# Kernel tuning notes

Measured on AMD Instinct MI355X. Metric: run time of the kernel, lower is better.

The kernel has to match this reference:

```python
import jax, jax.numpy as jnp
import numpy as np

EPS = 1e-5  # torch default for InstanceNorm2d and BatchNorm2d
B, C, H, W = 16, 128, 8192, 1


def _instance_norm(x):
    # normalize over spatial dims (H, W) per sample, per channel; affine=False (torch default)
    mean = jnp.mean(x, axis=(2, 3), keepdims=True)
    var = jnp.var(x, axis=(2, 3), keepdims=True)
    return (x - mean) * jax.lax.rsqrt(var + EPS)


def _batch_norm(x, gamma, beta):
    # training-mode batch norm: stats over (B, H, W) per channel, affine transform
    mean = jnp.mean(x, axis=(0, 2, 3), keepdims=True)
    var = jnp.var(x, axis=(0, 2, 3), keepdims=True)
    xn = (x - mean) * jax.lax.rsqrt(var + EPS)
    return xn * gamma[None, :, None, None] + beta[None, :, None, None]


def _block(x, g, be, w, b):
    # InstanceNorm -> BatchNorm -> ReLU -> 1x1 Conv
    x = jax.nn.relu(_batch_norm(_instance_norm(x), g, be))
    return jnp.einsum('bchw,oc->bohw', x, w) + b[None, :, None, None]


def setup_inputs() -> dict:
    key = jax.random.key(0)
    ks = jax.random.split(key, 6)
    return {
        'Correlation_feats': jax.random.normal(ks[0], (B, C, H, W), jnp.float32),
        'Coherence_residual_feats': jax.random.normal(ks[1], (B, C, H, W), jnp.float32),
        'feats': jax.random.normal(ks[2], (B, C, H, W), jnp.float32),
        'fc_w': jax.random.normal(ks[3], (2 * C,), jnp.float32) * 0.05,
        'fc_b': jnp.zeros((1,), jnp.float32),
        'w1': jax.random.normal(ks[4], (C, C), jnp.float32) * (1.0 / np.sqrt(C)),
        'b1': jnp.zeros((C,), jnp.float32),
        'g1': jnp.ones((C,), jnp.float32),
        'be1': jnp.zeros((C,), jnp.float32),
        'w2': jax.random.normal(ks[5], (C, C), jnp.float32) * (1.0 / np.sqrt(C)),
        'b2': jnp.zeros((C,), jnp.float32),
        'g2': jnp.ones((C,), jnp.float32),
        'be2': jnp.zeros((C,), jnp.float32),
    }


def reference(Correlation_feats, Coherence_residual_feats, feats,
              fc_w, fc_b, w1, b1, g1, be1, w2, b2, g2, be2):
    # pre_defined_alpha is None branch: alpha = sigmoid(fc(cat(Corr, Coh)))
    cat = jnp.concatenate([Correlation_feats, Coherence_residual_feats], axis=1)  # [B,2C,H,W]
    logit = jnp.einsum('bchw,c->bhw', cat, fc_w)[:, None, :, :] + fc_b[0]  # [B,1,H,W]
    alpha = jax.nn.sigmoid(logit)
    agg = Correlation_feats - alpha * feats
    x = _block(agg, g1, be1, w1, b1)
    x = _block(x, g2, be2, w2, b2)
    return x
```

## Files before the change

kernel.cpp:

```cpp
#include <hip/hip_runtime.h>

#define NB 16
#define NC 128
#define NH 8192
#define EPSN 1e-5f

typedef __attribute__((ext_vector_type(8))) short short8;
typedef __attribute__((ext_vector_type(4))) float f32x4;

__device__ inline unsigned short f2bf(float f) {
  unsigned int u = __builtin_bit_cast(unsigned int, f);
  u = u + 0x7FFFu + ((u >> 16) & 1u);
  return (unsigned short)(u >> 16);
}

__global__ __launch_bounds__(256) void alpha_kernel(
    const float* __restrict__ corr, const float* __restrict__ coh,
    const float* __restrict__ fcw, const float* __restrict__ fcb,
    float* __restrict__ alpha) {
  int idx = blockIdx.x * 256 + threadIdx.x;
  int b = idx >> 13;
  int h = idx & (NH - 1);
  const float* pc = corr + ((size_t)b * NC) * NH + h;
  const float* ph = coh + ((size_t)b * NC) * NH + h;
  float a0 = 0.f, a1 = 0.f, a2 = 0.f, a3 = 0.f;
#pragma unroll 8
  for (int c = 0; c < NC; c += 4) {
    a0 = fmaf(pc[(size_t)(c + 0) * NH], fcw[c + 0], a0);
    a1 = fmaf(pc[(size_t)(c + 1) * NH], fcw[c + 1], a1);
    a2 = fmaf(pc[(size_t)(c + 2) * NH], fcw[c + 2], a2);
    a3 = fmaf(pc[(size_t)(c + 3) * NH], fcw[c + 3], a3);
  }
#pragma unroll 8
  for (int c = 0; c < NC; c += 4) {
    a0 = fmaf(ph[(size_t)(c + 0) * NH], fcw[NC + c + 0], a0);
    a1 = fmaf(ph[(size_t)(c + 1) * NH], fcw[NC + c + 1], a1);
    a2 = fmaf(ph[(size_t)(c + 2) * NH], fcw[NC + c + 2], a2);
    a3 = fmaf(ph[(size_t)(c + 3) * NH], fcw[NC + c + 3], a3);
  }
  float l = (a0 + a1) + (a2 + a3) + fcb[0];
  alpha[idx] = 1.0f / (1.0f + __expf(-l));
}

__global__ __launch_bounds__(256) void agg_kernel(
    const float* __restrict__ corr, const float* __restrict__ feats,
    const float* __restrict__ alpha, float* __restrict__ agg,
    float* __restrict__ stats) {
  int blk = blockIdx.x;
  int chunk = blk & 3;
  int bc = blk >> 2;
  int b = bc >> 7;
  size_t base = (size_t)bc * NH + chunk * 2048;
  const float* pa = alpha + (size_t)b * NH + chunk * 2048;
  int t = threadIdx.x;
  float s = 0.f, q = 0.f;
#pragma unroll
  for (int r = 0; r < 2; ++r) {
    int off = r * 1024 + t * 4;
    float4 cv = *(const float4*)(corr + base + off);
    float4 fv = *(const float4*)(feats + base + off);
    float4 av = *(const float4*)(pa + off);
    float4 g;
    g.x = cv.x - av.x * fv.x;
    g.y = cv.y - av.y * fv.y;
    g.z = cv.z - av.z * fv.z;
    g.w = cv.w - av.w * fv.w;
    *(float4*)(agg + base + off) = g;
    s += (g.x + g.y) + (g.z + g.w);
    q = fmaf(g.x, g.x, q);
    q = fmaf(g.y, g.y, q);
    q = fmaf(g.z, g.z, q);
    q = fmaf(g.w, g.w, q);
  }
#pragma unroll
  for (int m = 32; m >= 1; m >>= 1) {
    s += __shfl_xor(s, m);
    q += __shfl_xor(q, m);
  }
  __shared__ float red[8];
  int wid = t >> 6;
  if ((t & 63) == 0) {
    red[wid * 2] = s;
    red[wid * 2 + 1] = q;
  }
  __syncthreads();
  if (t == 0) {
    float S = (red[0] + red[2]) + (red[4] + red[6]);
    float Q = (red[1] + red[3]) + (red[5] + red[7]);
    atomicAdd(&stats[bc * 2], S);
    atomicAdd(&stats[bc * 2 + 1], Q);
  }
}

__global__ void finalize_kernel(const float* __restrict__ stats,
                                const float* __restrict__ g,
                                const float* __restrict__ be,
                                float* __restrict__ scale,
                                float* __restrict__ shift) {
  int c = threadIdx.x;
  float mean[NB], rstd[NB];
  float bnacc = 0.f;
#pragma unroll
  for (int b = 0; b < NB; ++b) {
    float s = stats[(b * NC + c) * 2];
    float q = stats[(b * NC + c) * 2 + 1];
    float m = s * (1.f / NH);
    float v = fmaxf(q * (1.f / NH) - m * m, 0.f);
    float r = rsqrtf(v + EPSN);
    mean[b] = m;
    rstd[b] = r;
    bnacc += v * r * r;
  }
  float bnr = rsqrtf(bnacc * (1.f / NB) + EPSN);
  float gc = g[c], bec = be[c];
#pragma unroll
  for (int b = 0; b < NB; ++b) {
    float sc = rstd[b] * bnr * gc;
    scale[b * NC + c] = sc;
    shift[b * NC + c] = fmaf(-mean[b], sc, bec);
  }
}

template <bool DOSTATS>
__global__ __launch_bounds__(256) void conv_mfma_kernel(
    const float* X, const float* __restrict__ scale,
    const float* __restrict__ shift, const float* __restrict__ W,
    const float* __restrict__ bias, float* Out, float* __restrict__ stats) {
  __shared__ __align__(16) unsigned short sXf[8192];
  __shared__ float ssum[NC], ssq[NC];
  const int t = threadIdx.x;
  const int b = blockIdx.x >> 5;
  const int hbase = (blockIdx.x & 31) << 8;
  const int lane = t & 63;
  const int wv = t >> 6;
  const int wo = wv >> 1;
  const int wh = wv & 1;

  if (DOSTATS && t < NC) { ssum[t] = 0.f; ssq[t] = 0.f; }

  const int cb = (t >> 4) << 3;
  const int hq = t & 15;
  const int fragw = ((hq >> 2) << 2) + (cb >> 5);
  const int sub0 = (((cb >> 3) & 3) << 4) + ((hq & 3) << 2);
  const unsigned swz = ((unsigned)(sub0 >> 3)) << 4;
  const unsigned br = ((unsigned)(lane << 4)) ^ (((unsigned)(lane >> 3)) << 4);

  const float* Xb = X + ((size_t)(b * NC) << 13);
  float* Ob = Out + ((size_t)(b * NC) << 13);

  float4 xv[8];
#pragma unroll
  for (int p = 0; p < 8; ++p)
    xv[p] = *(const float4*)(Xb + ((size_t)(cb + p) << 13) + hbase + hq * 4);

  float scv[8], shv[8];
#pragma unroll
  for (int p = 0; p < 8; ++p) {
    scv[p] = scale[b * NC + cb + p];
    shv[p] = shift[b * NC + cb + p];
  }

  short8 wfr[4][4];
  {
    const int orow = wo * 64 + (lane & 15);
    const int cbw = 8 * (lane >> 4);
#pragma unroll
    for (int m = 0; m < 4; ++m) {
#pragma unroll
      for (int k = 0; k < 4; ++k) {
        const float* p = W + (orow + m * 16) * NC + k * 32 + cbw;
        float4 lo = *(const float4*)p;
        float4 hi = *(const float4*)(p + 4);
        union { short8 s; unsigned short u[8]; } fr;
        fr.u[0] = f2bf(lo.x); fr.u[1] = f2bf(lo.y);
        fr.u[2] = f2bf(lo.z); fr.u[3] = f2bf(lo.w);
        fr.u[4] = f2bf(hi.x); fr.u[5] = f2bf(hi.y);
        fr.u[6] = f2bf(hi.z); fr.u[7] = f2bf(hi.w);
        wfr[m][k] = fr.s;
      }
    }
  }

  float as_[4][4], aq_[4][4];
  if (DOSTATS) {
#pragma unroll
    for (int m = 0; m < 4; ++m)
#pragma unroll
      for (int r = 0; r < 4; ++r) { as_[m][r] = 0.f; aq_[m][r] = 0.f; }
  }

  const int og = (lane >> 4) << 2;
  const int hcol = lane & 15;

  for (int tt = 0; tt < 4; ++tt) {
#pragma unroll
    for (int r = 0; r < 4; ++r) {
      union { short8 s; unsigned short u[8]; } pk;
#pragma unroll
      for (int p = 0; p < 8; ++p) {
        float v = (r == 0) ? xv[p].x : (r == 1) ? xv[p].y : (r == 2) ? xv[p].z : xv[p].w;
        pk.u[p] = f2bf(fmaxf(fmaf(v, scv[p], shv[p]), 0.f));
      }
      unsigned addr = ((unsigned)(fragw << 10)) + ((((unsigned)(sub0 + r)) << 4) ^ swz);
      *(short8*)((char*)sXf + addr) = pk.s;
    }
    if (tt < 3) {
#pragma unroll
      for (int p = 0; p < 8; ++p)
        xv[p] = *(const float4*)(Xb + ((size_t)(cb + p) << 13) + hbase +
                                 (tt + 1) * 64 + hq * 4);
    }
    __syncthreads();

    f32x4 acc[4][2];
#pragma unroll
    for (int m = 0; m < 4; ++m) {
      acc[m][0] = (f32x4){0.f, 0.f, 0.f, 0.f};
      acc[m][1] = (f32x4){0.f, 0.f, 0.f, 0.f};
    }
#pragma unroll
    for (int k = 0; k < 4; ++k) {
      short8 x0 = *(const short8*)((char*)sXf + (((wh * 2 + 0) * 4 + k) << 10) + br);
      short8 x1 = *(const short8*)((char*)sXf + (((wh * 2 + 1) * 4 + k) << 10) + br);
#pragma unroll
      for (int m = 0; m < 4; ++m) {
        acc[m][0] = __builtin_amdgcn_mfma_f32_16x16x32_bf16(wfr[m][k], x0, acc[m][0], 0, 0, 0);
        acc[m][1] = __builtin_amdgcn_mfma_f32_16x16x32_bf16(wfr[m][k], x1, acc[m][1], 0, 0, 0);
      }
    }

    const int ha = hbase + tt * 64 + wh * 32 + hcol;
#pragma unroll
    for (int m = 0; m < 4; ++m) {
      int obase = wo * 64 + m * 16 + og;
#pragma unroll
      for (int r = 0; r < 4; ++r) {
        int o = obase + r;
        float bv = bias[o];
        float v0 = acc[m][0][r] + bv;
        float v1 = acc[m][1][r] + bv;
        float* po = Ob + ((size_t)o << 13);
        po[ha] = v0;
        po[ha + 16] = v1;
        if (DOSTATS) {
          as_[m][r] += v0 + v1;
          aq_[m][r] = fmaf(v0, v0, fmaf(v1, v1, aq_[m][r]));
        }
      }
    }
    __syncthreads();
  }

  if (DOSTATS) {
#pragma unroll
    for (int m = 0; m < 4; ++m) {
#pragma unroll
      for (int r = 0; r < 4; ++r) {
        float s = as_[m][r], q = aq_[m][r];
#pragma unroll
        for (int mm = 1; mm <= 8; mm <<= 1) {
          s += __shfl_xor(s, mm);
          q += __shfl_xor(q, mm);
        }
        if (hcol == 0) {
          int o = wo * 64 + m * 16 + og + r;
          atomicAdd(&ssum[o], s);
          atomicAdd(&ssq[o], q);
        }
      }
    }
    __syncthreads();
    if (t < NC) {
      atomicAdd(&stats[(b * NC + t) * 2], ssum[t]);
      atomicAdd(&stats[(b * NC + t) * 2 + 1], ssq[t]);
    }
  }
}

extern "C" void kernel_launch(void* const* d_in, const int* in_sizes, int n_in,
                              void* d_out, int out_size, void* d_ws,
                              size_t ws_size, hipStream_t stream) {
  const float* corr = (const float*)d_in[0];
  const float* coh = (const float*)d_in[1];
  const float* feats = (const float*)d_in[2];
  const float* fcw = (const float*)d_in[3];
  const float* fcb = (const float*)d_in[4];
  const float* w1 = (const float*)d_in[5];
  const float* b1 = (const float*)d_in[6];
  const float* g1 = (const float*)d_in[7];
  const float* be1 = (const float*)d_in[8];
  const float* w2 = (const float*)d_in[9];
  const float* b2 = (const float*)d_in[10];
  const float* g2 = (const float*)d_in[11];
  const float* be2 = (const float*)d_in[12];

  float* out = (float*)d_out;
  float* ws = (float*)d_ws;
  float* alphab = ws;
  float* stats1 = alphab + 131072;
  float* stats2 = stats1 + 4096;
  float* scale1 = stats2 + 4096;
  float* shift1 = scale1 + 2048;
  float* scale2 = shift1 + 2048;
  float* shift2 = scale2 + 2048;

  hipMemsetAsync(stats1, 0, 8192 * sizeof(float), stream);
  alpha_kernel<<<512, 256, 0, stream>>>(corr, coh, fcw, fcb, alphab);
  agg_kernel<<<8192, 256, 0, stream>>>(corr, feats, alphab, out, stats1);
  finalize_kernel<<<1, 128, 0, stream>>>(stats1, g1, be1, scale1, shift1);
  conv_mfma_kernel<true><<<512, 256, 0, stream>>>(out, scale1, shift1, w1, b1,
                                                  out, stats2);
  finalize_kernel<<<1, 128, 0, stream>>>(stats2, g2, be2, scale2, shift2);
  conv_mfma_kernel<false><<<512, 256, 0, stream>>>(out, scale2, shift2, w2, b2,
                                                   out, nullptr);
}
```

Measured before the change: 132.8 us.

## Fuse alpha and aggregation kernels, reuse corr in registers, double conv grid

```diff
diff --git a/kernel.cpp b/kernel.cpp
--- a/kernel.cpp
+++ b/kernel.cpp
@@ -14,81 +14,73 @@
   return (unsigned short)(u >> 16);
 }
 
-__global__ __launch_bounds__(256) void alpha_kernel(
+__global__ __launch_bounds__(256) void alphaagg_kernel(
     const float* __restrict__ corr, const float* __restrict__ coh,
-    const float* __restrict__ fcw, const float* __restrict__ fcb,
-    float* __restrict__ alpha) {
-  int idx = blockIdx.x * 256 + threadIdx.x;
-  int b = idx >> 13;
-  int h = idx & (NH - 1);
-  const float* pc = corr + ((size_t)b * NC) * NH + h;
-  const float* ph = coh + ((size_t)b * NC) * NH + h;
-  float a0 = 0.f, a1 = 0.f, a2 = 0.f, a3 = 0.f;
-#pragma unroll 8
-  for (int c = 0; c < NC; c += 4) {
-    a0 = fmaf(pc[(size_t)(c + 0) * NH], fcw[c + 0], a0);
-    a1 = fmaf(pc[(size_t)(c + 1) * NH], fcw[c + 1], a1);
-    a2 = fmaf(pc[(size_t)(c + 2) * NH], fcw[c + 2], a2);
-    a3 = fmaf(pc[(size_t)(c + 3) * NH], fcw[c + 3], a3);
-  }
-#pragma unroll 8
-  for (int c = 0; c < NC; c += 4) {
-    a0 = fmaf(ph[(size_t)(c + 0) * NH], fcw[NC + c + 0], a0);
-    a1 = fmaf(ph[(size_t)(c + 1) * NH], fcw[NC + c + 1], a1);
-    a2 = fmaf(ph[(size_t)(c + 2) * NH], fcw[NC + c + 2], a2);
-    a3 = fmaf(ph[(size_t)(c + 3) * NH], fcw[NC + c + 3], a3);
-  }
-  float l = (a0 + a1) + (a2 + a3) + fcb[0];
-  alpha[idx] = 1.0f / (1.0f + __expf(-l));
-}
-
-__global__ __launch_bounds__(256) void agg_kernel(
-    const float* __restrict__ corr, const float* __restrict__ feats,
-    const float* __restrict__ alpha, float* __restrict__ agg,
+    const float* __restrict__ feats, const float* __restrict__ fcw,
+    const float* __restrict__ fcb, float* __restrict__ agg,
     float* __restrict__ stats) {
-  int blk = blockIdx.x;
-  int chunk = blk & 3;
-  int bc = blk >> 2;
-  int b = bc >> 7;
-  size_t base = (size_t)bc * NH + chunk * 2048;
-  const float* pa = alpha + (size_t)b * NH + chunk * 2048;
-  int t = threadIdx.x;
-  float s = 0.f, q = 0.f;
-#pragma unroll
-  for (int r = 0; r < 2; ++r) {
-    int off = r * 1024 + t * 4;
-    float4 cv = *(const float4*)(corr + base + off);
-    float4 fv = *(const float4*)(feats + base + off);
-    float4 av = *(const float4*)(pa + off);
+  __shared__ float plog[8][128];
+  __shared__ float salpha[128];
+  const int t = threadIdx.x;
+  const int b = blockIdx.x >> 6;
+  const int h0 = (blockIdx.x & 63) << 7;
+  const int cpart = t >> 5;
+  const int hq = t & 31;
+  const int hoff = h0 + hq * 4;
+
+  float fw0[16], fw1[16];
+#pragma unroll
+  for (int k = 0; k < 4; ++k) {
+    *(float4*)&fw0[k * 4] = *(const float4*)(fcw + cpart * 16 + k * 4);
+    *(float4*)&fw1[k * 4] = *(const float4*)(fcw + NC + cpart * 16 + k * 4);
+  }
+
+  float4 cv[16];
+  float4 lg = {0.f, 0.f, 0.f, 0.f};
+#pragma unroll
+  for (int cc = 0; cc < 16; ++cc) {
+    int c = cpart * 16 + cc;
+    float4 cr = *(const float4*)(corr + ((size_t)(b * NC + c) << 13) + hoff);
+    float4 ch = *(const float4*)(coh + ((size_t)(b * NC + c) << 13) + hoff);
+    cv[cc] = cr;
+    lg.x = fmaf(cr.x, fw0[cc], fmaf(ch.x, fw1[cc], lg.x));
+    lg.y = fmaf(cr.y, fw0[cc], fmaf(ch.y, fw1[cc], lg.y));
+    lg.z = fmaf(cr.z, fw0[cc], fmaf(ch.z, fw1[cc], lg.z));
+    lg.w = fmaf(cr.w, fw0[cc], fmaf(ch.w, fw1[cc], lg.w));
+  }
+  *(float4*)&plog[cpart][hq * 4] = lg;
+  __syncthreads();
+
+  if (t < 128) {
+    float l = fcb[0];
+#pragma unroll
+    for (int p = 0; p < 8; ++p) l += plog[p][t];
+    salpha[t] = 1.0f / (1.0f + __expf(-l));
+  }
+  __syncthreads();
+
+  const float4 av = *(const float4*)&salpha[hq * 4];
+#pragma unroll
+  for (int cc = 0; cc < 16; ++cc) {
+    int c = cpart * 16 + cc;
+    float4 fv = *(const float4*)(feats + ((size_t)(b * NC + c) << 13) + hoff);
     float4 g;
-    g.x = cv.x - av.x * fv.x;
-    g.y = cv.y - av.y * fv.y;
-    g.z = cv.z - av.z * fv.z;
-    g.w = cv.w - av.w * fv.w;
-    *(float4*)(agg + base + off) = g;
-    s += (g.x + g.y) + (g.z + g.w);
-    q = fmaf(g.x, g.x, q);
-    q = fmaf(g.y, g.y, q);
-    q = fmaf(g.z, g.z, q);
-    q = fmaf(g.w, g.w, q);
-  }
-#pragma unroll
-  for (int m = 32; m >= 1; m >>= 1) {
-    s += __shfl_xor(s, m);
-    q += __shfl_xor(q, m);
-  }
-  __shared__ float red[8];
-  int wid = t >> 6;
-  if ((t & 63) == 0) {
-    red[wid * 2] = s;
-    red[wid * 2 + 1] = q;
-  }
-  __syncthreads();
-  if (t == 0) {
-    float S = (red[0] + red[2]) + (red[4] + red[6]);
-    float Q = (red[1] + red[3]) + (red[5] + red[7]);
-    atomicAdd(&stats[bc * 2], S);
-    atomicAdd(&stats[bc * 2 + 1], Q);
+    g.x = cv[cc].x - av.x * fv.x;
+    g.y = cv[cc].y - av.y * fv.y;
+    g.z = cv[cc].z - av.z * fv.z;
+    g.w = cv[cc].w - av.w * fv.w;
+    *(float4*)(agg + ((size_t)(b * NC + c) << 13) + hoff) = g;
+    float s = (g.x + g.y) + (g.z + g.w);
+    float q = fmaf(g.x, g.x, fmaf(g.y, g.y, fmaf(g.z, g.z, g.w * g.w)));
+#pragma unroll
+    for (int m = 1; m <= 16; m <<= 1) {
+      s += __shfl_xor(s, m);
+      q += __shfl_xor(q, m);
+    }
+    if (hq == 0) {
+      atomicAdd(&stats[(b * NC + c) * 2], s);
+      atomicAdd(&stats[(b * NC + c) * 2 + 1], q);
+    }
   }
 }
 
@@ -129,8 +121,8 @@
   __shared__ __align__(16) unsigned short sXf[8192];
   __shared__ float ssum[NC], ssq[NC];
   const int t = threadIdx.x;
-  const int b = blockIdx.x >> 5;
-  const int hbase = (blockIdx.x & 31) << 8;
+  const int b = blockIdx.x >> 6;
+  const int hbase = (blockIdx.x & 63) << 7;
   const int lane = t & 63;
   const int wv = t >> 6;
   const int wo = wv >> 1;
@@ -192,7 +184,7 @@
   const int og = (lane >> 4) << 2;
   const int hcol = lane & 15;
 
-  for (int tt = 0; tt < 4; ++tt) {
+  for (int tt = 0; tt < 2; ++tt) {
 #pragma unroll
     for (int r = 0; r < 4; ++r) {
       union { short8 s; unsigned short u[8]; } pk;
@@ -204,7 +196,7 @@
       unsigned addr = ((unsigned)(fragw << 10)) + ((((unsigned)(sub0 + r)) << 4) ^ swz);
       *(short8*)((char*)sXf + addr) = pk.s;
     }
-    if (tt < 3) {
+    if (tt < 1) {
 #pragma unroll
       for (int p = 0; p < 8; ++p)
         xv[p] = *(const float4*)(Xb + ((size_t)(cb + p) << 13) + hbase +
@@ -296,8 +288,7 @@
 
   float* out = (float*)d_out;
   float* ws = (float*)d_ws;
-  float* alphab = ws;
-  float* stats1 = alphab + 131072;
+  float* stats1 = ws;
   float* stats2 = stats1 + 4096;
   float* scale1 = stats2 + 4096;
   float* shift1 = scale1 + 2048;
@@ -305,12 +296,12 @@
   float* shift2 = scale2 + 2048;
 
   hipMemsetAsync(stats1, 0, 8192 * sizeof(float), stream);
-  alpha_kernel<<<512, 256, 0, stream>>>(corr, coh, fcw, fcb, alphab);
-  agg_kernel<<<8192, 256, 0, stream>>>(corr, feats, alphab, out, stats1);
+  alphaagg_kernel<<<1024, 256, 0, stream>>>(corr, coh, feats, fcw, fcb, out,
+                                            stats1);
   finalize_kernel<<<1, 128, 0, stream>>>(stats1, g1, be1, scale1, shift1);
-  conv_mfma_kernel<true><<<512, 256, 0, stream>>>(out, scale1, shift1, w1, b1,
-                                                  out, stats2);
+  conv_mfma_kernel<true><<<1024, 256, 0, stream>>>(out, scale1, shift1, w1, b1,
+                                                   out, stats2);
   finalize_kernel<<<1, 128, 0, stream>>>(stats2, g2, be2, scale2, shift2);
-  conv_mfma_kernel<false><<<512, 256, 0, stream>>>(out, scale2, shift2, w2, b2,
-                                                   out, nullptr);
-}
+  conv_mfma_kernel<false><<<1024, 256, 0, stream>>>(out, scale2, shift2, w2,
+                                                    b2, out, nullptr);
+}
```

New measurement: 143.9 us. 1.08x slower.

## Split alpha channel reduction across warps and halve conv tile per block

Applied to the files above, without the earlier changes.

```diff
diff --git a/kernel.cpp b/kernel.cpp
--- a/kernel.cpp
+++ b/kernel.cpp
@@ -14,32 +14,37 @@
   return (unsigned short)(u >> 16);
 }
 
-__global__ __launch_bounds__(256) void alpha_kernel(
+__global__ __launch_bounds__(1024) void alpha_kernel(
     const float* __restrict__ corr, const float* __restrict__ coh,
     const float* __restrict__ fcw, const float* __restrict__ fcb,
     float* __restrict__ alpha) {
-  int idx = blockIdx.x * 256 + threadIdx.x;
-  int b = idx >> 13;
-  int h = idx & (NH - 1);
-  const float* pc = corr + ((size_t)b * NC) * NH + h;
-  const float* ph = coh + ((size_t)b * NC) * NH + h;
+  __shared__ float part[4][256];
+  const int t = threadIdx.x;
+  const int b = blockIdx.x >> 5;
+  const int h0 = (blockIdx.x & 31) << 8;
+  const int w = t >> 6;
+  const int csub = w >> 2;
+  const int px = ((w & 3) << 6) + (t & 63);
+
+  const float* base = (csub < 2) ? corr : coh;
+  const int c0 = (csub & 1) << 6;
+  const float* p = base + ((size_t)(b * NC + c0) << 13) + h0 + px;
+  const float* fw = fcw + csub * 64;
+
   float a0 = 0.f, a1 = 0.f, a2 = 0.f, a3 = 0.f;
 #pragma unroll 8
-  for (int c = 0; c < NC; c += 4) {
-    a0 = fmaf(pc[(size_t)(c + 0) * NH], fcw[c + 0], a0);
-    a1 = fmaf(pc[(size_t)(c + 1) * NH], fcw[c + 1], a1);
-    a2 = fmaf(pc[(size_t)(c + 2) * NH], fcw[c + 2], a2);
-    a3 = fmaf(pc[(size_t)(c + 3) * NH], fcw[c + 3], a3);
-  }
-#pragma unroll 8
-  for (int c = 0; c < NC; c += 4) {
-    a0 = fmaf(ph[(size_t)(c + 0) * NH], fcw[NC + c + 0], a0);
-    a1 = fmaf(ph[(size_t)(c + 1) * NH], fcw[NC + c + 1], a1);
-    a2 = fmaf(ph[(size_t)(c + 2) * NH], fcw[NC + c + 2], a2);
-    a3 = fmaf(ph[(size_t)(c + 3) * NH], fcw[NC + c + 3], a3);
-  }
-  float l = (a0 + a1) + (a2 + a3) + fcb[0];
-  alpha[idx] = 1.0f / (1.0f + __expf(-l));
+  for (int j = 0; j < 64; j += 4) {
+    a0 = fmaf(p[(size_t)(j + 0) << 13], fw[j + 0], a0);
+    a1 = fmaf(p[(size_t)(j + 1) << 13], fw[j + 1], a1);
+    a2 = fmaf(p[(size_t)(j + 2) << 13], fw[j + 2], a2);
+    a3 = fmaf(p[(size_t)(j + 3) << 13], fw[j + 3], a3);
+  }
+  part[csub][px] = (a0 + a1) + (a2 + a3);
+  __syncthreads();
+  if (t < 256) {
+    float l = (part[0][t] + part[1][t]) + (part[2][t] + part[3][t]) + fcb[0];
+    alpha[b * NH + h0 + t] = 1.0f / (1.0f + __expf(-l));
+  }
 }
 
 __global__ __launch_bounds__(256) void agg_kernel(
@@ -129,8 +134,8 @@
   __shared__ __align__(16) unsigned short sXf[8192];
   __shared__ float ssum[NC], ssq[NC];
   const int t = threadIdx.x;
-  const int b = blockIdx.x >> 5;
-  const int hbase = (blockIdx.x & 31) << 8;
+  const int b = blockIdx.x >> 6;
+  const int hbase = (blockIdx.x & 63) << 7;
   const int lane = t & 63;
   const int wv = t >> 6;
   const int wo = wv >> 1;
@@ -192,7 +197,7 @@
   const int og = (lane >> 4) << 2;
   const int hcol = lane & 15;
 
-  for (int tt = 0; tt < 4; ++tt) {
+  for (int tt = 0; tt < 2; ++tt) {
 #pragma unroll
     for (int r = 0; r < 4; ++r) {
       union { short8 s; unsigned short u[8]; } pk;
@@ -204,7 +209,7 @@
       unsigned addr = ((unsigned)(fragw << 10)) + ((((unsigned)(sub0 + r)) << 4) ^ swz);
       *(short8*)((char*)sXf + addr) = pk.s;
     }
-    if (tt < 3) {
+    if (tt < 1) {
 #pragma unroll
       for (int p = 0; p < 8; ++p)
         xv[p] = *(const float4*)(Xb + ((size_t)(cb + p) << 13) + hbase +
@@ -305,12 +310,12 @@
   float* shift2 = scale2 + 2048;
 
   hipMemsetAsync(stats1, 0, 8192 * sizeof(float), stream);
-  alpha_kernel<<<512, 256, 0, stream>>>(corr, coh, fcw, fcb, alphab);
+  alpha_kernel<<<512, 1024, 0, stream>>>(corr, coh, fcw, fcb, alphab);
   agg_kernel<<<8192, 256, 0, stream>>>(corr, feats, alphab, out, stats1);
   finalize_kernel<<<1, 128, 0, stream>>>(stats1, g1, be1, scale1, shift1);
-  conv_mfma_kernel<true><<<512, 256, 0, stream>>>(out, scale1, shift1, w1, b1,
-                                                  out, stats2);
+  conv_mfma_kernel<true><<<1024, 256, 0, stream>>>(out, scale1, shift1, w1, b1,
+                                                   out, stats2);
   finalize_kernel<<<1, 128, 0, stream>>>(stats2, g2, be2, scale2, shift2);
-  conv_mfma_kernel<false><<<512, 256, 0, stream>>>(out, scale2, shift2, w2, b2,
-                                                   out, nullptr);
-}
+  conv_mfma_kernel<false><<<1024, 256, 0, stream>>>(out, scale2, shift2, w2,
+                                                    b2, out, nullptr);
+}
```

Result: slower. 142.1 us (+7.0%).
